# Kernel tuning notes

Measured on AMD Instinct MI355X. Metric: run time of the kernel, lower is better.

The kernel has to match this reference:

```python
import jax, jax.numpy as jnp
import numpy as np

N, B, D = 8, 4096, 1024
LOG_2PI = np.float32(np.log(2.0 * np.pi))


def setup_inputs() -> dict:
    key = jax.random.key(0)
    k1, k2 = jax.random.split(key)
    means = jax.random.normal(k1, (N, B, D), dtype=jnp.float32)
    logsigmas = jax.random.normal(k2, (N, B, D), dtype=jnp.float32)
    return {"means": means, "logsigmas": logsigmas}


def reference(means, logsigmas):
    # Sequential product of diagonal Gaussians.
    # Original builds DxD diag matrices + MVN log_prob; mathematically this is
    # purely elementwise over D plus a sum for the log-normalizer.
    m0, lv0 = means[0], logsigmas[0]
    lz0 = jnp.zeros(means.shape[1], dtype=means.dtype)

    def step(carry, inp):
        m1, lv1, lz = carry          # prior mean, log-variance, accumulated log_z
        m2, lv2 = inp                # next component
        v1 = jnp.exp(lv1)
        v2 = jnp.exp(lv2)
        iv1 = 1.0 / v1
        iv2 = 1.0 / v2
        cvar = 1.0 / (iv1 + iv2)              # combined variance (diag of C)
        cmean = cvar * (m1 * iv1 + m2 * iv2)  # combined mean
        s = v1 + v2 + 1e-6                    # covariance of the normalizer Gaussian
        # MVN(m2, diag(s)).log_prob(m1) == sum of univariate normal log-pdfs
        log_z = -0.5 * jnp.sum((m1 - m2) ** 2 / s + jnp.log(s) + LOG_2PI, axis=-1)
        return (cmean, jnp.log(cvar), lz + log_z), None

    (post_mean, post_logvar, log_z_total), _ = jax.lax.scan(
        step, (m0, lv0, lz0), (means[1:], logsigmas[1:])
    )
    return post_mean, post_logvar, log_z_total
```

## Files before the change

kernel.cpp:

```cpp
#include <hip/hip_runtime.h>
#include <math.h>

#define NN 8
#define BB 4096
#define DD 1024
#define LOG_2PI 1.8378770664093453f


__global__ __launch_bounds__(256) void mpc_kernel(
    const float* __restrict__ means,
    const float* __restrict__ logsig,
    float* __restrict__ out_mean,
    float* __restrict__ out_logvar,
    float* __restrict__ out_logz)
{
    const int b = blockIdx.x;
    const int t = threadIdx.x;
    const int wave = t >> 6;
    const int lane = t & 63;
    const size_t rowoff = (size_t)b * DD + (size_t)t * 4;
    const size_t plane = (size_t)BB * DD;

    float4 M[NN], L[NN];
#pragma unroll
    for (int n = 0; n < NN; ++n) {
        M[n] = *(const float4*)(means  + (size_t)n * plane + rowoff);
        L[n] = *(const float4*)(logsig + (size_t)n * plane + rowoff);
    }
    __builtin_amdgcn_sched_barrier(0);

    float m1[4], v1[4], iv1[4];
    {
        float m[4] = {M[0].x, M[0].y, M[0].z, M[0].w};
        float l[4] = {L[0].x, L[0].y, L[0].z, L[0].w};
#pragma unroll
        for (int j = 0; j < 4; ++j) {
            m1[j]  = m[j];
            v1[j]  = __expf(l[j]);
            iv1[j] = __expf(-l[j]);
        }
    }

    float z = 0.0f;

#pragma unroll
    for (int n = 1; n < NN; ++n) {
        float m2[4] = {M[n].x, M[n].y, M[n].z, M[n].w};
        float l2[4] = {L[n].x, L[n].y, L[n].z, L[n].w};
#pragma unroll
        for (int j = 0; j < 4; ++j) {
            float v2  = __expf(l2[j]);
            float iv2 = __expf(-l2[j]);
            float s   = v1[j] + v2 + 1e-6f;
            float diff = m1[j] - m2[j];
            z += diff * diff * __builtin_amdgcn_rcpf(s) + __logf(s);
            float iv_new = iv1[j] + iv2;
            float cvar   = __builtin_amdgcn_rcpf(iv_new);
            m1[j]  = cvar * (m1[j] * iv1[j] + m2[j] * iv2);
            v1[j]  = cvar;
            iv1[j] = iv_new;
        }
    }

    float4 om = make_float4(m1[0], m1[1], m1[2], m1[3]);
    float4 ol = make_float4(__logf(v1[0]), __logf(v1[1]),
                            __logf(v1[2]), __logf(v1[3]));
    *(float4*)(out_mean + rowoff)   = om;
    *(float4*)(out_logvar + rowoff) = ol;

#pragma unroll
    for (int o = 32; o > 0; o >>= 1)
        z += __shfl_down(z, o, 64);

    __shared__ float sz[4];
    if (lane == 0) sz[wave] = z;
    __syncthreads();
    if (t == 0) {
        float total = sz[0] + sz[1] + sz[2] + sz[3];
        out_logz[b] = -0.5f * (total + (float)((NN - 1) * DD) * LOG_2PI);
    }
}

extern "C" void kernel_launch(void* const* d_in, const int* in_sizes, int n_in,
                              void* d_out, int out_size, void* d_ws, size_t ws_size,
                              hipStream_t stream) {
    const float* means  = (const float*)d_in[0];
    const float* logsig = (const float*)d_in[1];
    float* out = (float*)d_out;
    float* out_mean   = out;
    float* out_logvar = out + (size_t)BB * DD;
    float* out_logz   = out + 2 * (size_t)BB * DD;
    mpc_kernel<<<BB, 256, 0, stream>>>(means, logsig, out_mean, out_logvar, out_logz);
}
```

Baseline: 296.3 us.

## Assign one row per wave and double-buffer plane loads across the scan

Measured after the change: 291.8 us. No clear change (-1.5%).

```diff
diff --git a/kernel.cpp b/kernel.cpp
--- a/kernel.cpp
+++ b/kernel.cpp
@@ -7,6 +7,8 @@
 #define LOG_2PI 1.8378770664093453f
 
 
+typedef float f32x4 __attribute__((ext_vector_type(4)));
+
 __global__ __launch_bounds__(256) void mpc_kernel(
     const float* __restrict__ means,
     const float* __restrict__ logsig,
@@ -14,71 +16,80 @@
     float* __restrict__ out_logvar,
     float* __restrict__ out_logz)
 {
-    const int b = blockIdx.x;
-    const int t = threadIdx.x;
+    const int t    = threadIdx.x;
     const int wave = t >> 6;
     const int lane = t & 63;
-    const size_t rowoff = (size_t)b * DD + (size_t)t * 4;
-    const size_t plane = (size_t)BB * DD;
+    const int row  = (blockIdx.x << 2) + wave;
+    const size_t plane   = (size_t)BB * DD;
+    const size_t rowbase = (size_t)row * DD;
+    const int off = lane * 4;
 
-    float4 M[NN], L[NN];
+    f32x4 bm[2][4], bl[2][4];
+
+#pragma unroll
+    for (int k = 0; k < 4; ++k) {
+        bm[0][k] = *(const f32x4*)(means  + rowbase + k * 256 + off);
+        bl[0][k] = *(const f32x4*)(logsig + rowbase + k * 256 + off);
+    }
+
+    float m1[16], v1[16], iv1[16];
+    float z = 0.0f;
+
 #pragma unroll
     for (int n = 0; n < NN; ++n) {
-        M[n] = *(const float4*)(means  + (size_t)n * plane + rowoff);
-        L[n] = *(const float4*)(logsig + (size_t)n * plane + rowoff);
-    }
-    __builtin_amdgcn_sched_barrier(0);
+        if (n + 1 < NN) {
+            const size_t pb = (size_t)(n + 1) * plane + rowbase;
+#pragma unroll
+            for (int k = 0; k < 4; ++k) {
+                bm[(n + 1) & 1][k] = *(const f32x4*)(means  + pb + k * 256 + off);
+                bl[(n + 1) & 1][k] = *(const f32x4*)(logsig + pb + k * 256 + off);
+            }
+        }
+        __builtin_amdgcn_sched_barrier(0);
 
-    float m1[4], v1[4], iv1[4];
-    {
-        float m[4] = {M[0].x, M[0].y, M[0].z, M[0].w};
-        float l[4] = {L[0].x, L[0].y, L[0].z, L[0].w};
 #pragma unroll
-        for (int j = 0; j < 4; ++j) {
-            m1[j]  = m[j];
-            v1[j]  = __expf(l[j]);
-            iv1[j] = __expf(-l[j]);
+        for (int k = 0; k < 4; ++k) {
+            const float mk[4] = {bm[n & 1][k].x, bm[n & 1][k].y,
+                                 bm[n & 1][k].z, bm[n & 1][k].w};
+            const float lk[4] = {bl[n & 1][k].x, bl[n & 1][k].y,
+                                 bl[n & 1][k].z, bl[n & 1][k].w};
+#pragma unroll
+            for (int j = 0; j < 4; ++j) {
+                const int e = k * 4 + j;
+                if (n == 0) {
+                    m1[e]  = mk[j];
+                    v1[e]  = __expf(lk[j]);
+                    iv1[e] = __expf(-lk[j]);
+                } else {
+                    float v2   = __expf(lk[j]);
+                    float iv2  = __expf(-lk[j]);
+                    float s    = v1[e] + v2 + 1e-6f;
+                    float d    = m1[e] - mk[j];
+                    z += d * d * __builtin_amdgcn_rcpf(s) + __logf(s);
+                    float ivn  = iv1[e] + iv2;
+                    float cv   = __builtin_amdgcn_rcpf(ivn);
+                    m1[e]  = cv * (m1[e] * iv1[e] + mk[j] * iv2);
+                    v1[e]  = cv;
+                    iv1[e] = ivn;
+                }
+            }
         }
     }
 
-    float z = 0.0f;
-
 #pragma unroll
-    for (int n = 1; n < NN; ++n) {
-        float m2[4] = {M[n].x, M[n].y, M[n].z, M[n].w};
-        float l2[4] = {L[n].x, L[n].y, L[n].z, L[n].w};
-#pragma unroll
-        for (int j = 0; j < 4; ++j) {
-            float v2  = __expf(l2[j]);
-            float iv2 = __expf(-l2[j]);
-            float s   = v1[j] + v2 + 1e-6f;
-            float diff = m1[j] - m2[j];
-            z += diff * diff * __builtin_amdgcn_rcpf(s) + __logf(s);
-            float iv_new = iv1[j] + iv2;
-            float cvar   = __builtin_amdgcn_rcpf(iv_new);
-            m1[j]  = cvar * (m1[j] * iv1[j] + m2[j] * iv2);
-            v1[j]  = cvar;
-            iv1[j] = iv_new;
-        }
+    for (int k = 0; k < 4; ++k) {
+        f32x4 om = {m1[k*4+0], m1[k*4+1], m1[k*4+2], m1[k*4+3]};
+        f32x4 ol = {__logf(v1[k*4+0]), __logf(v1[k*4+1]),
+                    __logf(v1[k*4+2]), __logf(v1[k*4+3])};
+        __builtin_nontemporal_store(om, (f32x4*)(out_mean   + rowbase + k * 256 + off));
+        __builtin_nontemporal_store(ol, (f32x4*)(out_logvar + rowbase + k * 256 + off));
     }
-
-    float4 om = make_float4(m1[0], m1[1], m1[2], m1[3]);
-    float4 ol = make_float4(__logf(v1[0]), __logf(v1[1]),
-                            __logf(v1[2]), __logf(v1[3]));
-    *(float4*)(out_mean + rowoff)   = om;
-    *(float4*)(out_logvar + rowoff) = ol;
 
 #pragma unroll
     for (int o = 32; o > 0; o >>= 1)
         z += __shfl_down(z, o, 64);
-
-    __shared__ float sz[4];
-    if (lane == 0) sz[wave] = z;
-    __syncthreads();
-    if (t == 0) {
-        float total = sz[0] + sz[1] + sz[2] + sz[3];
-        out_logz[b] = -0.5f * (total + (float)((NN - 1) * DD) * LOG_2PI);
-    }
+    if (lane == 0)
+        out_logz[row] = -0.5f * (z + (float)((NN - 1) * DD) * LOG_2PI);
 }
 
 extern "C" void kernel_launch(void* const* d_in, const int* in_sizes, int n_in,
@@ -90,5 +101,5 @@
     float* out_mean   = out;
     float* out_logvar = out + (size_t)BB * DD;
     float* out_logz   = out + 2 * (size_t)BB * DD;
-    mpc_kernel<<<BB, 256, 0, stream>>>(means, logsig, out_mean, out_logvar, out_logz);
+    mpc_kernel<<<BB / 4, 256, 0, stream>>>(means, logsig, out_mean, out_logvar, out_logz);
 }
```

## Issue all loads via inline asm with staged vmcnt waits and nontemporal stores

Applied to the files above, without the earlier changes.

Result: no change. 299.1 us (+0.9%).

```diff
diff --git a/kernel.cpp b/kernel.cpp
--- a/kernel.cpp
+++ b/kernel.cpp
@@ -7,6 +7,33 @@
 #define LOG_2PI 1.8378770664093453f
 
 
+typedef float f32x4 __attribute__((ext_vector_type(4)));
+
+#define GLD(dst, sp) \
+    asm volatile("global_load_dwordx4 %0, %1, %2" : "=v"(dst) : "v"(voff), "s"(sp))
+
+#define VWAIT(imm, a, b) \
+    asm volatile("s_waitcnt vmcnt(" #imm ")" : "+v"(a), "+v"(b))
+
+#define STEP(Mn, Ln)                                            \
+    do {                                                        \
+        _Pragma("unroll")                                       \
+        for (int j = 0; j < 4; ++j) {                           \
+            float mj  = Mn[j];                                  \
+            float lj  = Ln[j];                                  \
+            float v2  = __expf(lj);                             \
+            float iv2 = __expf(-lj);                            \
+            float v1e = __builtin_amdgcn_rcpf(iv1[j]);          \
+            float s   = v1e + v2 + 1e-6f;                       \
+            float d   = m1[j] - mj;                             \
+            z += d * d * __builtin_amdgcn_rcpf(s) + __logf(s);  \
+            float ivn = iv1[j] + iv2;                           \
+            float cv  = __builtin_amdgcn_rcpf(ivn);             \
+            m1[j]  = cv * (m1[j] * iv1[j] + mj * iv2);          \
+            iv1[j] = ivn;                                       \
+        }                                                       \
+    } while (0)
+
 __global__ __launch_bounds__(256) void mpc_kernel(
     const float* __restrict__ means,
     const float* __restrict__ logsig,
@@ -14,59 +41,57 @@
     float* __restrict__ out_logvar,
     float* __restrict__ out_logz)
 {
-    const int b = blockIdx.x;
-    const int t = threadIdx.x;
+    const int t    = threadIdx.x;
     const int wave = t >> 6;
     const int lane = t & 63;
-    const size_t rowoff = (size_t)b * DD + (size_t)t * 4;
+    const int row  = blockIdx.x;
     const size_t plane = (size_t)BB * DD;
+    const unsigned voff = ((unsigned)row << 12) + ((unsigned)wave << 10)
+                        + ((unsigned)lane << 4);
+    const int eoff = (row << 10) + (wave << 8) + (lane << 2);
 
-    float4 M[NN], L[NN];
-#pragma unroll
-    for (int n = 0; n < NN; ++n) {
-        M[n] = *(const float4*)(means  + (size_t)n * plane + rowoff);
-        L[n] = *(const float4*)(logsig + (size_t)n * plane + rowoff);
-    }
-    __builtin_amdgcn_sched_barrier(0);
+    const float* a0 = means;              const float* b0 = logsig;
+    const float* a1 = means + 1 * plane;  const float* b1 = logsig + 1 * plane;
+    const float* a2 = means + 2 * plane;  const float* b2 = logsig + 2 * plane;
+    const float* a3 = means + 3 * plane;  const float* b3 = logsig + 3 * plane;
+    const float* a4 = means + 4 * plane;  const float* b4 = logsig + 4 * plane;
+    const float* a5 = means + 5 * plane;  const float* b5 = logsig + 5 * plane;
+    const float* a6 = means + 6 * plane;  const float* b6 = logsig + 6 * plane;
+    const float* a7 = means + 7 * plane;  const float* b7 = logsig + 7 * plane;
 
-    float m1[4], v1[4], iv1[4];
-    {
-        float m[4] = {M[0].x, M[0].y, M[0].z, M[0].w};
-        float l[4] = {L[0].x, L[0].y, L[0].z, L[0].w};
-#pragma unroll
-        for (int j = 0; j < 4; ++j) {
-            m1[j]  = m[j];
-            v1[j]  = __expf(l[j]);
-            iv1[j] = __expf(-l[j]);
-        }
-    }
+    f32x4 M0, M1, M2, M3, M4, M5, M6, M7;
+    f32x4 L0, L1, L2, L3, L4, L5, L6, L7;
+    GLD(M0, a0); GLD(L0, b0);
+    GLD(M1, a1); GLD(L1, b1);
+    GLD(M2, a2); GLD(L2, b2);
+    GLD(M3, a3); GLD(L3, b3);
+    GLD(M4, a4); GLD(L4, b4);
+    GLD(M5, a5); GLD(L5, b5);
+    GLD(M6, a6); GLD(L6, b6);
+    GLD(M7, a7); GLD(L7, b7);
 
+    float m1[4], iv1[4];
     float z = 0.0f;
 
+    VWAIT(14, M0, L0);
 #pragma unroll
-    for (int n = 1; n < NN; ++n) {
-        float m2[4] = {M[n].x, M[n].y, M[n].z, M[n].w};
-        float l2[4] = {L[n].x, L[n].y, L[n].z, L[n].w};
-#pragma unroll
-        for (int j = 0; j < 4; ++j) {
-            float v2  = __expf(l2[j]);
-            float iv2 = __expf(-l2[j]);
-            float s   = v1[j] + v2 + 1e-6f;
-            float diff = m1[j] - m2[j];
-            z += diff * diff * __builtin_amdgcn_rcpf(s) + __logf(s);
-            float iv_new = iv1[j] + iv2;
-            float cvar   = __builtin_amdgcn_rcpf(iv_new);
-            m1[j]  = cvar * (m1[j] * iv1[j] + m2[j] * iv2);
-            v1[j]  = cvar;
-            iv1[j] = iv_new;
-        }
+    for (int j = 0; j < 4; ++j) {
+        m1[j]  = M0[j];
+        iv1[j] = __expf(-L0[j]);
     }
+    VWAIT(12, M1, L1); STEP(M1, L1);
+    VWAIT(10, M2, L2); STEP(M2, L2);
+    VWAIT(8,  M3, L3); STEP(M3, L3);
+    VWAIT(6,  M4, L4); STEP(M4, L4);
+    VWAIT(4,  M5, L5); STEP(M5, L5);
+    VWAIT(2,  M6, L6); STEP(M6, L6);
+    VWAIT(0,  M7, L7); STEP(M7, L7);
 
-    float4 om = make_float4(m1[0], m1[1], m1[2], m1[3]);
-    float4 ol = make_float4(__logf(v1[0]), __logf(v1[1]),
-                            __logf(v1[2]), __logf(v1[3]));
-    *(float4*)(out_mean + rowoff)   = om;
-    *(float4*)(out_logvar + rowoff) = ol;
+    f32x4 om = {m1[0], m1[1], m1[2], m1[3]};
+    f32x4 ol = {-__logf(iv1[0]), -__logf(iv1[1]),
+                -__logf(iv1[2]), -__logf(iv1[3])};
+    __builtin_nontemporal_store(om, (f32x4*)(out_mean   + eoff));
+    __builtin_nontemporal_store(ol, (f32x4*)(out_logvar + eoff));
 
 #pragma unroll
     for (int o = 32; o > 0; o >>= 1)
@@ -77,7 +102,7 @@
     __syncthreads();
     if (t == 0) {
         float total = sz[0] + sz[1] + sz[2] + sz[3];
-        out_logz[b] = -0.5f * (total + (float)((NN - 1) * DD) * LOG_2PI);
+        out_logz[row] = -0.5f * (total + (float)((NN - 1) * DD) * LOG_2PI);
     }
 }
 
```

## Use one thread per element with 1024-thread blocks and nontemporal stores

Applied to the files above, without the earlier changes.

Measured after the change: 295.9 us. No clear change (-0.1%).

```diff
diff --git a/kernel.cpp b/kernel.cpp
--- a/kernel.cpp
+++ b/kernel.cpp
@@ -7,77 +7,60 @@
 #define LOG_2PI 1.8378770664093453f
 
 
-__global__ __launch_bounds__(256) void mpc_kernel(
+__global__ __launch_bounds__(1024) void mpc_kernel(
     const float* __restrict__ means,
     const float* __restrict__ logsig,
     float* __restrict__ out_mean,
     float* __restrict__ out_logvar,
     float* __restrict__ out_logz)
 {
-    const int b = blockIdx.x;
-    const int t = threadIdx.x;
+    const int t    = threadIdx.x;
     const int wave = t >> 6;
     const int lane = t & 63;
-    const size_t rowoff = (size_t)b * DD + (size_t)t * 4;
+    const int row  = blockIdx.x;
+    const int e    = (row << 10) + t;
     const size_t plane = (size_t)BB * DD;
 
-    float4 M[NN], L[NN];
+    float M[NN], L[NN];
 #pragma unroll
     for (int n = 0; n < NN; ++n) {
-        M[n] = *(const float4*)(means  + (size_t)n * plane + rowoff);
-        L[n] = *(const float4*)(logsig + (size_t)n * plane + rowoff);
+        M[n] = means [(size_t)n * plane + e];
+        L[n] = logsig[(size_t)n * plane + e];
     }
     __builtin_amdgcn_sched_barrier(0);
 
-    float m1[4], v1[4], iv1[4];
-    {
-        float m[4] = {M[0].x, M[0].y, M[0].z, M[0].w};
-        float l[4] = {L[0].x, L[0].y, L[0].z, L[0].w};
+    float m1  = M[0];
+    float iv1 = __expf(-L[0]);
+    float z   = 0.0f;
 #pragma unroll
-        for (int j = 0; j < 4; ++j) {
-            m1[j]  = m[j];
-            v1[j]  = __expf(l[j]);
-            iv1[j] = __expf(-l[j]);
-        }
+    for (int n = 1; n < NN; ++n) {
+        float v2  = __expf(L[n]);
+        float iv2 = __expf(-L[n]);
+        float v1  = __builtin_amdgcn_rcpf(iv1);
+        float s   = v1 + v2 + 1e-6f;
+        float d   = m1 - M[n];
+        z += d * d * __builtin_amdgcn_rcpf(s) + __logf(s);
+        float ivn = iv1 + iv2;
+        float cv  = __builtin_amdgcn_rcpf(ivn);
+        m1  = cv * (m1 * iv1 + M[n] * iv2);
+        iv1 = ivn;
     }
 
-    float z = 0.0f;
-
-#pragma unroll
-    for (int n = 1; n < NN; ++n) {
-        float m2[4] = {M[n].x, M[n].y, M[n].z, M[n].w};
-        float l2[4] = {L[n].x, L[n].y, L[n].z, L[n].w};
-#pragma unroll
-        for (int j = 0; j < 4; ++j) {
-            float v2  = __expf(l2[j]);
-            float iv2 = __expf(-l2[j]);
-            float s   = v1[j] + v2 + 1e-6f;
-            float diff = m1[j] - m2[j];
-            z += diff * diff * __builtin_amdgcn_rcpf(s) + __logf(s);
-            float iv_new = iv1[j] + iv2;
-            float cvar   = __builtin_amdgcn_rcpf(iv_new);
-            m1[j]  = cvar * (m1[j] * iv1[j] + m2[j] * iv2);
-            v1[j]  = cvar;
-            iv1[j] = iv_new;
-        }
-    }
-
-    float4 om = make_float4(m1[0], m1[1], m1[2], m1[3]);
-    float4 ol = make_float4(__logf(v1[0]), __logf(v1[1]),
-                            __logf(v1[2]), __logf(v1[3]));
-    *(float4*)(out_mean + rowoff)   = om;
-    *(float4*)(out_logvar + rowoff) = ol;
+    __builtin_nontemporal_store(m1,           out_mean   + e);
+    __builtin_nontemporal_store(-__logf(iv1), out_logvar + e);
 
 #pragma unroll
     for (int o = 32; o > 0; o >>= 1)
         z += __shfl_down(z, o, 64);
 
-    __shared__ float sz[4];
+    __shared__ float sz[16];
     if (lane == 0) sz[wave] = z;
     __syncthreads();
     if (t == 0) {
-        float total = sz[0] + sz[1] + sz[2] + sz[3];
-        out_logz[b] = -0.5f * (total + (float)((NN - 1) * DD) * LOG_2PI);
+        float total = 0.0f;
+#pragma unroll
+        for (int w = 0; w < 16; ++w) total += sz[w];
+        out_logz[row] = -0.5f * (total + (float)((NN - 1) * DD) * LOG_2PI);
     }
 }
 
@@ -90,5 +73,5 @@
     float* out_mean   = out;
     float* out_logvar = out + (size_t)BB * DD;
     float* out_logz   = out + 2 * (size_t)BB * DD;
-    mpc_kernel<<<BB, 256, 0, stream>>>(means, logsig, out_mean, out_logvar, out_logz);
+    mpc_kernel<<<BB, 1024, 0, stream>>>(means, logsig, out_mean, out_logvar, out_logz);
 }
```
